# Performance work log

Hardware: AMD Instinct MI355X
Metric: run time of the kernel (lower is better)

Reference implementation:

```python
import jax, jax.numpy as jnp
import numpy as np

B, S, H, L = 128, 512, 1024, 9

def setup_inputs() -> dict:
    key = jax.random.key(0)
    k1, k2, k3 = jax.random.split(key, 3)
    sequence_output = jax.random.normal(k1, (B, S, H), dtype=jnp.float32)
    W = jax.random.normal(k2, (H, L), dtype=jnp.float32) * 0.02
    b = jnp.zeros((L,), dtype=jnp.float32)
    valid_ids = jax.random.randint(k3, (B, S), 0, 2, dtype=jnp.int32)
    return {"sequence_output": sequence_output, "W": W, "b": b, "valid_ids": valid_ids}

def reference(sequence_output, W, b, valid_ids):
    # Stable-sort each row by (1 - valid): valid tokens compacted to the front
    # preserving order, invalid slots pushed to the back and zeroed (pad).
    order = jnp.argsort(1 - valid_ids, axis=1, stable=True)          # [B, S]
    gathered = jnp.take_along_axis(sequence_output, order[:, :, None], axis=1)  # [B,S,H]
    mask = jnp.take_along_axis(valid_ids, order, axis=1).astype(sequence_output.dtype)
    valid_output = gathered * mask[:, :, None]
    # Dropout is identity at inference (training=False default).
    logits = jax.nn.softmax(jnp.einsum('bsh,hl->bsl', valid_output, W) + b, axis=-1)
    return logits
```

## Files before the change

### kernel.cpp

```cpp
#include <hip/hip_runtime.h>

#define B_ 128
#define S_ 512
#define H_ 1024
#define L_ 9
#define NB 512

__global__ __launch_bounds__(256) void prep_kernel(
    const int* __restrict__ valid, const float* __restrict__ bias,
    float* __restrict__ out, int* __restrict__ ws_src, int* __restrict__ ws_nv) {
    __shared__ int cnt[8];
    const int lane = threadIdx.x & 63;
    const int wv = threadIdx.x >> 6;
    const int b = blockIdx.x;
    const int* vrow = valid + (size_t)b * S_;

    int v0 = vrow[128 * wv + lane];
    int v1 = vrow[128 * wv + 64 + lane];
    unsigned long long m0 = __ballot(v0 != 0);
    unsigned long long m1 = __ballot(v1 != 0);
    if (lane == 0) { cnt[2 * wv] = __popcll(m0); cnt[2 * wv + 1] = __popcll(m1); }
    __syncthreads();

    int base0 = 0, total = 0;
#pragma unroll
    for (int k = 0; k < 8; ++k) {
        if (k < 2 * wv) base0 += cnt[k];
        total += cnt[k];
    }
    int base1 = base0 + cnt[2 * wv];
    if (v0) ws_src[b * S_ + base0 + __popcll(m0 & ((1ull << lane) - 1ull))] =
        128 * wv + lane;
    if (v1) ws_src[b * S_ + base1 + __popcll(m1 & ((1ull << lane) - 1ull))] =
        128 * wv + 64 + lane;
    if (threadIdx.x == 0) ws_nv[b] = total;

    float pv[L_];
    float mx = bias[0];
#pragma unroll
    for (int l = 1; l < L_; ++l) mx = fmaxf(mx, bias[l]);
    float s = 0.f;
#pragma unroll
    for (int l = 0; l < L_; ++l) { pv[l] = expf(bias[l] - mx); s += pv[l]; }
    float inv = 1.f / s;
#pragma unroll
    for (int l = 0; l < L_; ++l) pv[l] *= inv;
    for (int j = total + threadIdx.x; j < S_; j += 256) {
        float* op = out + ((size_t)b * S_ + j) * L_;
#pragma unroll
        for (int l = 0; l < L_; ++l) op[l] = pv[l];
    }
}

__global__ __launch_bounds__(256, 2) void gemm_kernel(
    const float* __restrict__ seq, const float* __restrict__ Wm,
    const float* __restrict__ bias, const int* __restrict__ ws_src,
    const int* __restrict__ ws_nv, float* __restrict__ out) {
    __shared__ __align__(16) float Wl[H_ * L_];
    __shared__ int offs[B_ + 1];
    __shared__ int srow[64], orow[64];

    const int tid = threadIdx.x;
    const int lane = tid & 63;
    const int wv = __builtin_amdgcn_readfirstlane(tid >> 6);
    const int hl = lane & 15;
    const int g = lane >> 4;

    if (tid < 64) {
        int s0 = ws_nv[lane], s1 = ws_nv[64 + lane];
#pragma unroll
        for (int d = 1; d < 64; d <<= 1) {
            int t0 = __shfl_up(s0, d, 64), t1 = __shfl_up(s1, d, 64);
            if (lane >= d) { s0 += t0; s1 += t1; }
        }
        int tot0 = __shfl(s0, 63, 64);
        offs[1 + lane] = s0;
        offs[65 + lane] = tot0 + s1;
        if (lane == 0) offs[0] = 0;
    }
    {
        const float4* Wg = (const float4*)Wm;
        float4* Wd = (float4*)Wl;
#pragma unroll
        for (int k = 0; k < 9; ++k) Wd[k * 256 + tid] = Wg[k * 256 + tid];
    }
    __syncthreads();

    const int total = offs[B_];
    const int chunk = (total + NB - 1) / NB;
    const int Gs = blockIdx.x * chunk;
    const int Ge = min(Gs + chunk, total);
    if (Gs >= Ge) return;

    for (int t0 = Gs; t0 < Ge; t0 += 64) {
        if (tid < 64) {
            int G = t0 + tid;
            int sa = -1, o = 0;
            if (G < Ge) {
                int lo = 0, hi = B_;
                while (hi - lo > 1) {
                    int mid = (lo + hi) >> 1;
                    if (offs[mid] <= G) lo = mid; else hi = mid;
                }
                int j = G - offs[lo];
                o = lo * S_ + j;
                sa = lo * S_ + ws_src[o];
            }
            srow[tid] = sa;
            orow[tid] = o;
        }
        __syncthreads();

        const float* rp[4];
#pragma unroll
        for (int s = 0; s < 4; ++s) {
            int sa = srow[16 * wv + 4 * s + g];
            rp[s] = seq + (size_t)(sa < 0 ? 0 : sa) * H_ + 4 * hl;
        }

        float acc[4][L_];
#pragma unroll
        for (int s = 0; s < 4; ++s)
#pragma unroll
            for (int l = 0; l < L_; ++l) acc[s][l] = 0.f;

#pragma unroll 2
        for (int it = 0; it < 16; ++it) {
            float4 xv0 = *(const float4*)(rp[0] + 64 * it);
            float4 xv1 = *(const float4*)(rp[1] + 64 * it);
            float4 xv2 = *(const float4*)(rp[2] + 64 * it);
            float4 xv3 = *(const float4*)(rp[3] + 64 * it);
            const float* wf = Wl + 36 * hl + 576 * it;
            float wr[36];
#pragma unroll
            for (int j = 0; j < 9; ++j)
                *(float4*)&wr[4 * j] = *(const float4*)(wf + 4 * j);
            float xk0[4] = {xv0.x, xv0.y, xv0.z, xv0.w};
            float xk1[4] = {xv1.x, xv1.y, xv1.z, xv1.w};
            float xk2[4] = {xv2.x, xv2.y, xv2.z, xv2.w};
            float xk3[4] = {xv3.x, xv3.y, xv3.z, xv3.w};
#pragma unroll
            for (int k = 0; k < 4; ++k)
#pragma unroll
                for (int l = 0; l < L_; ++l) {
                    float w = wr[9 * k + l];
                    acc[0][l] = fmaf(xk0[k], w, acc[0][l]);
                    acc[1][l] = fmaf(xk1[k], w, acc[1][l]);
                    acc[2][l] = fmaf(xk2[k], w, acc[2][l]);
                    acc[3][l] = fmaf(xk3[k], w, acc[3][l]);
                }
        }

#pragma unroll
        for (int m = 1; m < 16; m <<= 1)
#pragma unroll
            for (int s = 0; s < 4; ++s)
#pragma unroll
                for (int l = 0; l < L_; ++l)
                    acc[s][l] += __shfl_xor(acc[s][l], m);

        if (hl < 4) {
            float v[L_];
#pragma unroll
            for (int s = 0; s < 4; ++s)
                if (hl == s) {
#pragma unroll
                    for (int l = 0; l < L_; ++l) v[l] = acc[s][l];
                }
            int rw = 16 * wv + 4 * hl + g;
            if (srow[rw] >= 0) {
#pragma unroll
                for (int l = 0; l < L_; ++l) v[l] += bias[l];
                float mx = v[0];
#pragma unroll
                for (int l = 1; l < L_; ++l) mx = fmaxf(mx, v[l]);
                float s = 0.f;
#pragma unroll
                for (int l = 0; l < L_; ++l) {
                    v[l] = expf(v[l] - mx);
                    s += v[l];
                }
                float inv = 1.f / s;
                float* op = out + (size_t)orow[rw] * L_;
#pragma unroll
                for (int l = 0; l < L_; ++l) op[l] = v[l] * inv;
            }
        }
        __syncthreads();
    }
}

extern "C" void kernel_launch(void* const* d_in, const int* in_sizes, int n_in,
                              void* d_out, int out_size, void* d_ws, size_t ws_size,
                              hipStream_t stream) {
    const float* seq = (const float*)d_in[0];
    const float* W = (const float*)d_in[1];
    const float* bias = (const float*)d_in[2];
    const int* valid = (const int*)d_in[3];
    float* out = (float*)d_out;

    int* ws_src = (int*)d_ws;
    int* ws_nv = ws_src + B_ * S_;

    prep_kernel<<<dim3(B_), dim3(256), 0, stream>>>(valid, bias, out, ws_src, ws_nv);
    gemm_kernel<<<dim3(NB), dim3(256), 0, stream>>>(seq, W, bias, ws_src, ws_nv,
                                                    out);
}
```

Before: 34.37 us.

## Fuse compaction prep into GEMM kernel, recomputing offsets and source rows per block

Removes the separate prep kernel. Each block now counts the whole valid matrix itself to build per-batch offsets, writes its share of the pad-row softmax outputs, and finds source rows for its tile by ballot and bit-select over the affected valid rows. Seq loads and output stores become nontemporal. This saves a kernel launch and the workspace round trip, at the cost of every block redundantly reading the full 256KB valid array and doing extra scan work before the GEMM.

```diff
diff --git a/kernel.cpp b/kernel.cpp
--- a/kernel.cpp
+++ b/kernel.cpp
@@ -6,57 +6,25 @@
 #define L_ 9
 #define NB 512
 
-__global__ __launch_bounds__(256) void prep_kernel(
-    const int* __restrict__ valid, const float* __restrict__ bias,
-    float* __restrict__ out, int* __restrict__ ws_src, int* __restrict__ ws_nv) {
-    __shared__ int cnt[8];
-    const int lane = threadIdx.x & 63;
-    const int wv = threadIdx.x >> 6;
-    const int b = blockIdx.x;
-    const int* vrow = valid + (size_t)b * S_;
-
-    int v0 = vrow[128 * wv + lane];
-    int v1 = vrow[128 * wv + 64 + lane];
-    unsigned long long m0 = __ballot(v0 != 0);
-    unsigned long long m1 = __ballot(v1 != 0);
-    if (lane == 0) { cnt[2 * wv] = __popcll(m0); cnt[2 * wv + 1] = __popcll(m1); }
-    __syncthreads();
-
-    int base0 = 0, total = 0;
-#pragma unroll
-    for (int k = 0; k < 8; ++k) {
-        if (k < 2 * wv) base0 += cnt[k];
-        total += cnt[k];
-    }
-    int base1 = base0 + cnt[2 * wv];
-    if (v0) ws_src[b * S_ + base0 + __popcll(m0 & ((1ull << lane) - 1ull))] =
-        128 * wv + lane;
-    if (v1) ws_src[b * S_ + base1 + __popcll(m1 & ((1ull << lane) - 1ull))] =
-        128 * wv + 64 + lane;
-    if (threadIdx.x == 0) ws_nv[b] = total;
-
-    float pv[L_];
-    float mx = bias[0];
-#pragma unroll
-    for (int l = 1; l < L_; ++l) mx = fmaxf(mx, bias[l]);
-    float s = 0.f;
-#pragma unroll
-    for (int l = 0; l < L_; ++l) { pv[l] = expf(bias[l] - mx); s += pv[l]; }
-    float inv = 1.f / s;
-#pragma unroll
-    for (int l = 0; l < L_; ++l) pv[l] *= inv;
-    for (int j = total + threadIdx.x; j < S_; j += 256) {
-        float* op = out + ((size_t)b * S_ + j) * L_;
-#pragma unroll
-        for (int l = 0; l < L_; ++l) op[l] = pv[l];
-    }
+typedef float f32x4 __attribute__((ext_vector_type(4)));
+
+__device__ __forceinline__ int select_bit(unsigned long long m, int r) {
+    int pos = 0;
+#pragma unroll
+    for (int w = 32; w >= 1; w >>= 1) {
+        unsigned long long lowmask = ((1ull << w) - 1ull);
+        int c = __popcll(m & lowmask);
+        if (r >= c) { r -= c; m >>= w; pos += w; }
+    }
+    return pos;
 }
 
-__global__ __launch_bounds__(256, 2) void gemm_kernel(
+__global__ __launch_bounds__(256, 2) void fused_kernel(
     const float* __restrict__ seq, const float* __restrict__ Wm,
-    const float* __restrict__ bias, const int* __restrict__ ws_src,
-    const int* __restrict__ ws_nv, float* __restrict__ out) {
+    const float* __restrict__ bias, const int* __restrict__ valid,
+    float* __restrict__ out) {
     __shared__ __align__(16) float Wl[H_ * L_];
+    __shared__ int cnt[256];
     __shared__ int offs[B_ + 1];
     __shared__ int srow[64], orow[64];
 
@@ -66,8 +34,29 @@
     const int hl = lane & 15;
     const int g = lane >> 4;
 
+    {
+        const float4* Wg = (const float4*)Wm;
+        float4* Wd = (float4*)Wl;
+#pragma unroll
+        for (int k = 0; k < 9; ++k) Wd[k * 256 + tid] = Wg[k * 256 + tid];
+    }
+
+    {
+        const int4* vp =
+            (const int4*)(valid + (size_t)(tid >> 1) * S_ + (tid & 1) * 256);
+        int c = 0;
+#pragma unroll
+        for (int k = 0; k < 64; ++k) {
+            int4 v = vp[k];
+            c += (v.x != 0) + (v.y != 0) + (v.z != 0) + (v.w != 0);
+        }
+        cnt[tid] = c;
+    }
+    __syncthreads();
+
     if (tid < 64) {
-        int s0 = ws_nv[lane], s1 = ws_nv[64 + lane];
+        int s0 = cnt[2 * lane] + cnt[2 * lane + 1];
+        int s1 = cnt[128 + 2 * lane] + cnt[128 + 2 * lane + 1];
 #pragma unroll
         for (int d = 1; d < 64; d <<= 1) {
             int t0 = __shfl_up(s0, d, 64), t1 = __shfl_up(s1, d, 64);
@@ -78,15 +67,38 @@
         offs[65 + lane] = tot0 + s1;
         if (lane == 0) offs[0] = 0;
     }
-    {
-        const float4* Wg = (const float4*)Wm;
-        float4* Wd = (float4*)Wl;
-#pragma unroll
-        for (int k = 0; k < 9; ++k) Wd[k * 256 + tid] = Wg[k * 256 + tid];
-    }
     __syncthreads();
 
     const int total = offs[B_];
+
+    if (tid >= 64 && tid < 192) {
+        const int P = B_ * S_ - total;
+        const int padchunk = (P + NB - 1) / NB;
+        int pi = tid - 64;
+        int p = blockIdx.x * padchunk + pi;
+        if (pi < padchunk && p < P) {
+            int lo = 0, hi = B_;
+            while (hi - lo > 1) {
+                int mid = (lo + hi) >> 1;
+                if (mid * S_ - offs[mid] <= p) lo = mid; else hi = mid;
+            }
+            int nv = offs[lo + 1] - offs[lo];
+            int j = nv + (p - (lo * S_ - offs[lo]));
+            float pv[L_];
+            float mx = bias[0];
+#pragma unroll
+            for (int l = 1; l < L_; ++l) mx = fmaxf(mx, bias[l]);
+            float s = 0.f;
+#pragma unroll
+            for (int l = 0; l < L_; ++l) { pv[l] = expf(bias[l] - mx); s += pv[l]; }
+            float inv = 1.f / s;
+            float* op = out + ((size_t)lo * S_ + j) * L_;
+#pragma unroll
+            for (int l = 0; l < L_; ++l)
+                __builtin_nontemporal_store(pv[l] * inv, op + l);
+        }
+    }
+
     const int chunk = (total + NB - 1) / NB;
     const int Gs = blockIdx.x * chunk;
     const int Ge = min(Gs + chunk, total);
@@ -94,20 +106,37 @@
 
     for (int t0 = Gs; t0 < Ge; t0 += 64) {
         if (tid < 64) {
-            int G = t0 + tid;
-            int sa = -1, o = 0;
-            if (G < Ge) {
+            const int G = t0 + lane;
+            const bool act = G < Ge;
+            int bt = 0, jt = 0;
+            if (act) {
                 int lo = 0, hi = B_;
                 while (hi - lo > 1) {
                     int mid = (lo + hi) >> 1;
                     if (offs[mid] <= G) lo = mid; else hi = mid;
                 }
-                int j = G - offs[lo];
-                o = lo * S_ + j;
-                sa = lo * S_ + ws_src[o];
-            }
-            srow[tid] = sa;
-            orow[tid] = o;
+                bt = lo;
+                jt = G - offs[lo];
+            }
+            srow[lane] = -1;
+            orow[lane] = act ? bt * S_ + jt : 0;
+            int lastA = Ge - 1 - t0;
+            if (lastA > 63) lastA = 63;
+            const int blo = __shfl(bt, 0);
+            const int bhi = __shfl(bt, lastA);
+            for (int bb = blo; bb <= bhi; ++bb) {
+                const int* vrow = valid + (size_t)bb * S_;
+                int base = 0;
+#pragma unroll
+                for (int c = 0; c < 8; ++c) {
+                    int vv = vrow[c * 64 + lane];
+                    unsigned long long m = __ballot(vv != 0);
+                    int pc = __popcll(m);
+                    if (act && bt == bb && jt >= base && jt < base + pc)
+                        srow[lane] = bb * S_ + c * 64 + select_bit(m, jt - base);
+                    base += pc;
+                }
+            }
         }
         __syncthreads();
 
@@ -126,19 +155,19 @@
 
 #pragma unroll 2
         for (int it = 0; it < 16; ++it) {
-            float4 xv0 = *(const float4*)(rp[0] + 64 * it);
-            float4 xv1 = *(const float4*)(rp[1] + 64 * it);
-            float4 xv2 = *(const float4*)(rp[2] + 64 * it);
-            float4 xv3 = *(const float4*)(rp[3] + 64 * it);
+            f32x4 xv0 = __builtin_nontemporal_load((const f32x4*)(rp[0] + 64 * it));
+            f32x4 xv1 = __builtin_nontemporal_load((const f32x4*)(rp[1] + 64 * it));
+            f32x4 xv2 = __builtin_nontemporal_load((const f32x4*)(rp[2] + 64 * it));
+            f32x4 xv3 = __builtin_nontemporal_load((const f32x4*)(rp[3] + 64 * it));
             const float* wf = Wl + 36 * hl + 576 * it;
             float wr[36];
 #pragma unroll
             for (int j = 0; j < 9; ++j)
                 *(float4*)&wr[4 * j] = *(const float4*)(wf + 4 * j);
-            float xk0[4] = {xv0.x, xv0.y, xv0.z, xv0.w};
-            float xk1[4] = {xv1.x, xv1.y, xv1.z, xv1.w};
-            float xk2[4] = {xv2.x, xv2.y, xv2.z, xv2.w};
-            float xk3[4] = {xv3.x, xv3.y, xv3.z, xv3.w};
+            float xk0[4] = {xv0[0], xv0[1], xv0[2], xv0[3]};
+            float xk1[4] = {xv1[0], xv1[1], xv1[2], xv1[3]};
+            float xk2[4] = {xv2[0], xv2[1], xv2[2], xv2[3]};
+            float xk3[4] = {xv3[0], xv3[1], xv3[2], xv3[3]};
 #pragma unroll
             for (int k = 0; k < 4; ++k)
 #pragma unroll
@@ -183,7 +212,8 @@
                 float inv = 1.f / s;
                 float* op = out + (size_t)orow[rw] * L_;
 #pragma unroll
-                for (int l = 0; l < L_; ++l) op[l] = v[l] * inv;
+                for (int l = 0; l < L_; ++l)
+                    __builtin_nontemporal_store(v[l] * inv, op + l);
             }
         }
         __syncthreads();
@@ -199,10 +229,5 @@
     const int* valid = (const int*)d_in[3];
     float* out = (float*)d_out;
 
-    int* ws_src = (int*)d_ws;
-    int* ws_nv = ws_src + B_ * S_;
-
-    prep_kernel<<<dim3(B_), dim3(256), 0, stream>>>(valid, bias, out, ws_src, ws_nv);
-    gemm_kernel<<<dim3(NB), dim3(256), 0, stream>>>(seq, W, bias, ws_src, ws_nv,
-                                                    out);
+    fused_kernel<<<dim3(NB), dim3(256), 0, stream>>>(seq, W, bias, valid, out);
 }
```

Measured after the change: 50.62 us. +47.3%, slower.
